# Kernel tuning notes

Hardware: AMD Instinct MI355X
Metric: run time of the kernel (lower is better)

## Reference

```python
import jax, jax.numpy as jnp
import numpy as np

NEG_SLOPE = 0.01  # nn.LeakyReLU default
EM_DIM = 64

def setup_inputs() -> dict:
    key = jax.random.key(0)
    k1, k2, k3, k4, k5 = jax.random.split(key, 5)
    B, N, D = 4, 512, EM_DIM
    embeddings = jax.random.normal(k1, (B, N, D), dtype=jnp.float32)
    # att_W: Linear(D, D) -> weight [D, D], bias [D]
    W_w = jax.random.normal(k2, (D, D), dtype=jnp.float32) * (1.0 / np.sqrt(D))
    W_b = jax.random.normal(k3, (D,), dtype=jnp.float32) * 0.01
    # att_a: Linear(3D, 1) -> weight [3D], bias scalar
    a_w = jax.random.normal(k4, (3 * D,), dtype=jnp.float32) * (1.0 / np.sqrt(3 * D))
    a_b = jax.random.normal(k5, (1,), dtype=jnp.float32) * 0.01
    return {"embeddings": embeddings, "W_w": W_w, "W_b": W_b, "a_w": a_w, "a_b": a_b}

def reference(embeddings, W_w, W_b, a_w, a_b):
    # embeddings: [B, N, D]
    D = embeddings.shape[-1]
    # pairwise elementwise product: value[b,i,j,d] = e[b,i,d] * e[b,j,d]
    value = embeddings[:, :, None, :] * embeddings[:, None, :, :]  # [B,N,N,D]
    # att_W applied to (broadcast) query/key is row/col-constant -> compute once per node
    w_e = jnp.einsum('bnd,ed->bne', embeddings, W_w) + W_b   # [B,N,D] (= wq rows = wk cols)
    wv = jnp.einsum('bijd,ed->bije', value, W_w) + W_b       # [B,N,N,D]
    # att_a on concat(wq, wk, wv): split the weight vector into three D-chunks
    a_q, a_k, a_v = a_w[:D], a_w[D:2*D], a_w[2*D:]
    s_q = w_e @ a_q  # [B,N]
    s_k = w_e @ a_k  # [B,N]
    s = s_q[:, :, None] + s_k[:, None, :] + jnp.einsum('bije,e->bij', wv, a_v) + a_b[0]  # [B,N,N]
    s = jnp.where(s >= 0, s, NEG_SLOPE * s)  # LeakyReLU; dropout is identity in eval
    alphas = jax.nn.softmax(s, axis=-1)[..., None]  # [B,N,N,1]
    return alphas, value
```

## Files before the change

### kernel.cpp

```cpp
#include <hip/hip_runtime.h>

#define DD 64
#define NN 512
#define BB 4
#define NEG_SLOPE 0.01f

__global__ void precompute_kernel(const float* __restrict__ W_w,
                                  const float* __restrict__ W_b,
                                  const float* __restrict__ a_w,
                                  const float* __restrict__ a_b,
                                  float* __restrict__ ws) {
    int d = threadIdx.x;
    float cq = 0.f, ck = 0.f, cv = 0.f;
    for (int e = 0; e < DD; ++e) {
        float w = W_w[e * DD + d];
        cq = fmaf(a_w[e], w, cq);
        ck = fmaf(a_w[DD + e], w, ck);
        cv = fmaf(a_w[2 * DD + e], w, cv);
    }
    ws[d] = cq;
    ws[DD + d] = ck;
    ws[2 * DD + d] = cv;
    float p = W_b[d] * (a_w[d] + a_w[DD + d] + a_w[2 * DD + d]);
#pragma unroll
    for (int off = 32; off; off >>= 1) p += __shfl_down(p, off, 64);
    if (d == 0) ws[3 * DD] = p + a_b[0];
}

__global__ __launch_bounds__(256) void attn_row_kernel(
        const float* __restrict__ emb,
        const float* __restrict__ ws,
        float* __restrict__ out_alpha,
        float* __restrict__ out_value) {
    const int row = blockIdx.x;
    const int b = row >> 9;
    const int t = threadIdx.x;
    const int d4 = t & 15;
    const int jl = t >> 4;

    __shared__ float s_lds[NN];
    __shared__ float red[8];

    const float4* emb4 = (const float4*)emb;
    const float4 ei = emb4[(size_t)row * 16 + d4];
    const float4 cq = ((const float4*)ws)[d4];
    const float4 ck = ((const float4*)(ws + DD))[d4];
    const float4 cv = ((const float4*)(ws + 2 * DD))[d4];
    const float Cc = ws[3 * DD];

    const float4* embB = emb4 + (size_t)b * NN * 16;
    float4* val4 = (float4*)(out_value + (size_t)row * NN * DD);

    const float pq = ei.x * cq.x + ei.y * cq.y + ei.z * cq.z + ei.w * cq.w;

#pragma unroll 4
    for (int it = 0; it < NN / 16; ++it) {
        const int j = it * 16 + jl;
        const float4 ej = embB[j * 16 + d4];
        float4 p;
        p.x = ei.x * ej.x; p.y = ei.y * ej.y;
        p.z = ei.z * ej.z; p.w = ei.w * ej.w;
        val4[j * 16 + d4] = p;
        float v = p.x * cv.x + p.y * cv.y + p.z * cv.z + p.w * cv.w
                + ej.x * ck.x + ej.y * ck.y + ej.z * ck.z + ej.w * ck.w
                + pq;
        v += __shfl_xor(v, 1, 64);
        v += __shfl_xor(v, 2, 64);
        v += __shfl_xor(v, 4, 64);
        v += __shfl_xor(v, 8, 64);
        if (d4 == 0) {
            float s = v + Cc;
            s_lds[j] = (s >= 0.f) ? s : NEG_SLOPE * s;
        }
    }
    __syncthreads();

    float s0 = s_lds[t], s1 = s_lds[t + 256];
    float m = fmaxf(s0, s1);
#pragma unroll
    for (int off = 32; off; off >>= 1) m = fmaxf(m, __shfl_xor(m, off, 64));
    const int wid = t >> 6, lane = t & 63;
    if (lane == 0) red[wid] = m;
    __syncthreads();
    m = fmaxf(fmaxf(red[0], red[1]), fmaxf(red[2], red[3]));

    float e0 = expf(s0 - m), e1 = expf(s1 - m);
    float ps = e0 + e1;
#pragma unroll
    for (int off = 32; off; off >>= 1) ps += __shfl_xor(ps, off, 64);
    if (lane == 0) red[4 + wid] = ps;
    __syncthreads();
    const float inv = 1.f / (red[4] + red[5] + red[6] + red[7]);

    float* arow = out_alpha + (size_t)row * NN;
    arow[t] = e0 * inv;
    arow[t + 256] = e1 * inv;
}

extern "C" void kernel_launch(void* const* d_in, const int* in_sizes, int n_in,
                              void* d_out, int out_size, void* d_ws, size_t ws_size,
                              hipStream_t stream) {
    const float* emb = (const float*)d_in[0];
    const float* W_w = (const float*)d_in[1];
    const float* W_b = (const float*)d_in[2];
    const float* a_w = (const float*)d_in[3];
    const float* a_b = (const float*)d_in[4];
    float* ws = (float*)d_ws;

    float* out = (float*)d_out;
    float* out_alpha = out;
    float* out_value = out + (size_t)BB * NN * NN;

    precompute_kernel<<<1, 64, 0, stream>>>(W_w, W_b, a_w, a_b, ws);
    attn_row_kernel<<<BB * NN, 256, 0, stream>>>(emb, ws, out_alpha, out_value);
}
```

Measured before the change: 274.8 us.

## Split value write into separate nontemporal-store kernel and simplify score math

Splits the fused kernel into a pure value-output kernel that writes with nontemporal stores and an alpha kernel that computes only scores and softmax. The score dot product is folded algebraically into one precomputed vector (ei*cv+ck), so each iteration does a single 4-wide dot. The aim is to let the dominant 256MB value write stream at full bandwidth without shuffle and softmax work interleaved, at the cost of an extra kernel launch and re-reading embeddings.

```diff
diff --git a/kernel.cpp b/kernel.cpp
--- a/kernel.cpp
+++ b/kernel.cpp
@@ -4,6 +4,8 @@
 #define NN 512
 #define BB 4
 #define NEG_SLOPE 0.01f
+
+typedef float floatx4 __attribute__((ext_vector_type(4)));
 
 __global__ void precompute_kernel(const float* __restrict__ W_w,
                                   const float* __restrict__ W_b,
@@ -27,11 +29,33 @@
     if (d == 0) ws[3 * DD] = p + a_b[0];
 }
 
-__global__ __launch_bounds__(256) void attn_row_kernel(
+__global__ __launch_bounds__(256) void value_kernel(
+        const float* __restrict__ emb,
+        float* __restrict__ out_value) {
+    const int row = blockIdx.x;
+    const int b = row >> 9;
+    const int t = threadIdx.x;
+    const int d4 = t & 15;
+    const int jl = t >> 4;
+
+    const floatx4* emb4 = (const floatx4*)emb;
+    const floatx4 ei = emb4[(size_t)row * 16 + d4];
+    const floatx4* embB = emb4 + (size_t)b * NN * 16;
+    floatx4* val4 = (floatx4*)out_value + (size_t)row * NN * 16;
+
+#pragma unroll 8
+    for (int it = 0; it < NN / 16; ++it) {
+        const int j = it * 16 + jl;
+        const floatx4 ej = embB[j * 16 + d4];
+        const floatx4 p = ei * ej;
+        __builtin_nontemporal_store(p, &val4[j * 16 + d4]);
+    }
+}
+
+__global__ __launch_bounds__(256) void alpha_kernel(
         const float* __restrict__ emb,
         const float* __restrict__ ws,
-        float* __restrict__ out_alpha,
-        float* __restrict__ out_value) {
+        float* __restrict__ out_alpha) {
     const int row = blockIdx.x;
     const int b = row >> 9;
     const int t = threadIdx.x;
@@ -41,29 +65,23 @@
     __shared__ float s_lds[NN];
     __shared__ float red[8];
 
-    const float4* emb4 = (const float4*)emb;
-    const float4 ei = emb4[(size_t)row * 16 + d4];
-    const float4 cq = ((const float4*)ws)[d4];
-    const float4 ck = ((const float4*)(ws + DD))[d4];
-    const float4 cv = ((const float4*)(ws + 2 * DD))[d4];
+    const floatx4* emb4 = (const floatx4*)emb;
+    const floatx4 ei = emb4[(size_t)row * 16 + d4];
+    const floatx4 cq = ((const floatx4*)ws)[d4];
+    const floatx4 ck = ((const floatx4*)(ws + DD))[d4];
+    const floatx4 cv = ((const floatx4*)(ws + 2 * DD))[d4];
     const float Cc = ws[3 * DD];
 
-    const float4* embB = emb4 + (size_t)b * NN * 16;
-    float4* val4 = (float4*)(out_value + (size_t)row * NN * DD);
+    const floatx4* embB = emb4 + (size_t)b * NN * 16;
 
+    floatx4 cvec = ei * cv + ck;
     const float pq = ei.x * cq.x + ei.y * cq.y + ei.z * cq.z + ei.w * cq.w;
 
 #pragma unroll 4
     for (int it = 0; it < NN / 16; ++it) {
         const int j = it * 16 + jl;
-        const float4 ej = embB[j * 16 + d4];
-        float4 p;
-        p.x = ei.x * ej.x; p.y = ei.y * ej.y;
-        p.z = ei.z * ej.z; p.w = ei.w * ej.w;
-        val4[j * 16 + d4] = p;
-        float v = p.x * cv.x + p.y * cv.y + p.z * cv.z + p.w * cv.w
-                + ej.x * ck.x + ej.y * ck.y + ej.z * ck.z + ej.w * ck.w
-                + pq;
+        const floatx4 ej = embB[j * 16 + d4];
+        float v = ej.x * cvec.x + ej.y * cvec.y + ej.z * cvec.z + ej.w * cvec.w + pq;
         v += __shfl_xor(v, 1, 64);
         v += __shfl_xor(v, 2, 64);
         v += __shfl_xor(v, 4, 64);
@@ -111,6 +129,7 @@
     float* out_alpha = out;
     float* out_value = out + (size_t)BB * NN * NN;
 
+    value_kernel<<<BB * NN, 256, 0, stream>>>(emb, out_value);
     precompute_kernel<<<1, 64, 0, stream>>>(W_w, W_b, a_w, a_b, ws);
-    attn_row_kernel<<<BB * NN, 256, 0, stream>>>(emb, ws, out_alpha, out_value);
+    alpha_kernel<<<BB * NN, 256, 0, stream>>>(emb, ws, out_alpha);
 }
```

Measured after the change: 302.5 us. 10.1% more time.
